# Kernel tuning notes

Measured on AMD Instinct MI355X. Metric: run time of the kernel, lower is better.

The kernel has to match this reference:

```python
import jax, jax.numpy as jnp
import numpy as np

D_MODEL = 1024
NUM_HEADS = 16
HEAD_DIM = D_MODEL // NUM_HEADS


def setup_inputs() -> dict:
    key = jax.random.key(0)
    ks = jax.random.split(key, 5)
    B, S = 2, 2048
    x = jax.random.normal(ks[0], (B, S, D_MODEL), dtype=jnp.float32)
    # nn.Linear(d,d,bias=False): y = x @ W.T, W is [out,in]. Init ~ U(-1/sqrt(d), 1/sqrt(d)).
    lim = 1.0 / np.sqrt(D_MODEL)
    wq = jax.random.uniform(ks[1], (D_MODEL, D_MODEL), jnp.float32, -lim, lim)
    wk = jax.random.uniform(ks[2], (D_MODEL, D_MODEL), jnp.float32, -lim, lim)
    wv = jax.random.uniform(ks[3], (D_MODEL, D_MODEL), jnp.float32, -lim, lim)
    wo = jax.random.uniform(ks[4], (D_MODEL, D_MODEL), jnp.float32, -lim, lim)
    return {"x": x, "wq": wq, "wk": wk, "wv": wv, "wo": wo}


def reference(x, wq, wk, wv, wo):
    B, S, D = x.shape
    H, Hd = NUM_HEADS, HEAD_DIM
    scale = Hd ** 0.5
    # projections (torch Linear: x @ W.T), split heads -> [B,H,S,Hd]
    q = (x @ wq.T).reshape(B, S, H, Hd).transpose(0, 2, 1, 3)
    k = (x @ wk.T).reshape(B, S, H, Hd).transpose(0, 2, 1, 3)
    v = (x @ wv.T).reshape(B, S, H, Hd).transpose(0, 2, 1, 3)
    scores = jnp.einsum('bhqd,bhkd->bhqk', q, k) / scale  # [B,H,S,S]
    # causal mask: disallow j > i
    causal_mask = jnp.triu(jnp.ones((S, S), dtype=bool), k=1)
    scores = jnp.where(causal_mask, -jnp.inf, scores)
    attn = jax.nn.softmax(scores, axis=-1)
    out = jnp.einsum('bhqk,bhkd->bhqd', attn, v)
    out = out.transpose(0, 2, 1, 3).reshape(B, S, D)
    return out @ wo.T
```

## Files before the change

kernel.cpp:

```cpp
#include <hip/hip_runtime.h>

#define DEV __device__ __forceinline__

typedef __attribute__((ext_vector_type(4))) float f32x4;
typedef __attribute__((ext_vector_type(8))) __bf16 bf16x8;

typedef __attribute__((address_space(1))) const uint32_t gu32;
typedef __attribute__((address_space(3))) uint32_t su32;

DEV void gload16(const void* g, void* s) {
  __builtin_amdgcn_global_load_lds((gu32*)(uintptr_t)g,
                                   (su32*)(uint32_t)(uintptr_t)s, 16, 0, 0);
}

DEV ushort bfbits(float f) { return __builtin_bit_cast(ushort, (__bf16)f); }

DEV bf16x8 lds8(const ushort* p) {
  return __builtin_bit_cast(bf16x8, *(const uint4*)(p));
}

DEV void vmcnt0bar() {
  asm volatile("s_waitcnt vmcnt(0)" ::: "memory");
  __builtin_amdgcn_s_barrier();
}

__global__ void cvt_all(const float* __restrict__ x, const float* __restrict__ wq,
                        const float* __restrict__ wk, const float* __restrict__ wv,
                        const float* __restrict__ wo, ushort* __restrict__ xb,
                        ushort* __restrict__ wb) {
  int i = blockIdx.x * blockDim.x + threadIdx.x;
  const float* src; ushort* dst; float scl = 1.0f; int j;
  if (i < 1048576) { src = x; dst = xb; j = i; }
  else {
    int t = (i - 1048576) >> 18;
    j = (i - 1048576) & 262143;
    src = t == 0 ? wq : (t == 1 ? wk : (t == 2 ? wv : wo));
    dst = wb + t * 1048576;
    if (t == 0) scl = 0.18033688011f;
  }
  float4 v = ((const float4*)src)[j];
  ushort4 o;
  o.x = bfbits(v.x * scl); o.y = bfbits(v.y * scl);
  o.z = bfbits(v.z * scl); o.w = bfbits(v.w * scl);
  ((ushort4*)dst)[j] = o;
}

template <int NFR, int F32OUT>
DEV void gemm_core(const ushort* __restrict__ A, const ushort* __restrict__ W,
                   void* __restrict__ Cout, ushort* sA, ushort* sB) {
  const int tid = threadIdx.x;
  const int l = tid & 63, wv = tid >> 6;
  const int g = l >> 4, lan = l & 15;
  const int wr = wv >> 1, wc = wv & 1;
  const int brow = blockIdx.y * 128, bcol = blockIdx.x * (NFR * 32);
  const int ASZ = 128 * 32, BSZ = NFR * 32 * 32;

  f32x4 acc[4][NFR] = {};

  auto stage = [&](int buf, int k0) {
    ushort* dA = sA + buf * ASZ;
    ushort* dB = sB + buf * BSZ;
#pragma unroll
    for (int i = 0; i < 2; ++i) {
      int n = i * 256 + wv * 64 + l;
      int row = n >> 2, ss = n & 3, gs = (ss - (row >> 1)) & 3;
      gload16(A + (size_t)(brow + row) * 1024 + k0 + gs * 8,
              dA + (i * 256 + wv * 64) * 8);
    }
#pragma unroll
    for (int i = 0; i < NFR / 2; ++i) {
      int n = i * 256 + wv * 64 + l;
      int row = n >> 2, ss = n & 3, gs = (ss - (row >> 1)) & 3;
      gload16(W + (size_t)(bcol + row) * 1024 + k0 + gs * 8,
              dB + (i * 256 + wv * 64) * 8);
    }
  };

  auto compute = [&](int buf) {
    const ushort* cA = sA + buf * ASZ;
    const ushort* cB = sB + buf * BSZ;
    bf16x8 a[4], b[NFR];
#pragma unroll
    for (int fr = 0; fr < 4; ++fr) {
      int row = wr * 64 + fr * 16 + lan;
      a[fr] = lds8(cA + row * 32 + 8 * (((row >> 1) + g) & 3));
    }
#pragma unroll
    for (int fn = 0; fn < NFR; ++fn) {
      int row = wc * (NFR * 16) + fn * 16 + lan;
      b[fn] = lds8(cB + row * 32 + 8 * (((row >> 1) + g) & 3));
    }
    __builtin_amdgcn_s_setprio(1);
#pragma unroll
    for (int fr = 0; fr < 4; ++fr)
#pragma unroll
      for (int fn = 0; fn < NFR; ++fn)
        acc[fr][fn] = __builtin_amdgcn_mfma_f32_16x16x32_bf16(a[fr], b[fn], acc[fr][fn], 0, 0, 0);
    __builtin_amdgcn_s_setprio(0);
  };

  stage(0, 0);
  vmcnt0bar();
#pragma unroll 1
  for (int t = 0; t < 15; ++t) {
    stage(1, (2 * t + 1) * 32); compute(0); vmcnt0bar();
    stage(0, (2 * t + 2) * 32); compute(1); vmcnt0bar();
  }
  stage(1, 31 * 32); compute(0); vmcnt0bar();
  compute(1);

#pragma unroll
  for (int fr = 0; fr < 4; ++fr)
#pragma unroll
    for (int fn = 0; fn < NFR; ++fn)
#pragma unroll
      for (int r = 0; r < 4; ++r) {
        int row = brow + wr * 64 + fr * 16 + g * 4 + r;
        int col = bcol + wc * (NFR * 16) + fn * 16 + lan;
        if (F32OUT)
          ((float*)Cout)[(size_t)row * 1024 + col] = acc[fr][fn][r];
        else
          ((ushort*)Cout)[(size_t)row * 1024 + col] = bfbits(acc[fr][fn][r]);
      }
}

__global__ __launch_bounds__(256) void gemm_qkv(
    const ushort* __restrict__ X, const ushort* __restrict__ Wb,
    ushort* __restrict__ Q, ushort* __restrict__ K, ushort* __restrict__ V) {
  __shared__ __align__(16) ushort sA[2 * 128 * 32];
  __shared__ __align__(16) ushort sB[2 * 128 * 32];
  const ushort* W = Wb + (size_t)blockIdx.z * 1048576;
  ushort* C = blockIdx.z == 0 ? Q : (blockIdx.z == 1 ? K : V);
  gemm_core<4, 0>(X, W, (void*)C, sA, sB);
}

__global__ __launch_bounds__(256) void gemm_out(
    const ushort* __restrict__ AO, const ushort* __restrict__ Wo, float* __restrict__ C) {
  __shared__ __align__(16) ushort sA[2 * 128 * 32];
  __shared__ __align__(16) ushort sB[2 * 64 * 32];
  gemm_core<2, 1>(AO, Wo, (void*)C, sA, sB);
}

__global__ __launch_bounds__(256) void vt_kernel(const ushort* __restrict__ V,
                                                 ushort* __restrict__ Vt) {
  __shared__ __align__(16) ushort T[64 * 64];
  const int tid = threadIdx.x;
  const int stile = blockIdx.x, bh = blockIdx.y;
  const int b = bh >> 4, h = bh & 15;

#pragma unroll
  for (int i = 0; i < 2; ++i) {
    int m = i * 256 + tid;
    int s = m >> 3, dc = m & 7;
    uint4 v = *(const uint4*)(V + (size_t)(b * 2048 + stile * 64 + s) * 1024 + h * 64 + dc * 8);
    *(uint4*)(T + s * 64 + ((8 * dc) ^ (((s >> 3) & 7) << 3))) = v;
  }
  __syncthreads();

#pragma unroll
  for (int i = 0; i < 2; ++i) {
    int m = i * 256 + tid;
    int d = m >> 3, sb = m & 7;
    ushort tmp[8];
#pragma unroll
    for (int e = 0; e < 8; ++e)
      tmp[e] = T[(sb * 8 + e) * 64 + (d ^ (sb << 3))];
    uint4 o;
    o.x = (uint)tmp[0] | ((uint)tmp[1] << 16);
    o.y = (uint)tmp[2] | ((uint)tmp[3] << 16);
    o.z = (uint)tmp[4] | ((uint)tmp[5] << 16);
    o.w = (uint)tmp[6] | ((uint)tmp[7] << 16);
    *(uint4*)(Vt + ((size_t)bh * 64 + d) * 2048 + stile * 64 + sb * 8) = o;
  }
}

__global__ __launch_bounds__(256) void attn_fwd(
    const ushort* __restrict__ Qm, const ushort* __restrict__ Km,
    const ushort* __restrict__ Vt, ushort* __restrict__ AO) {
  __shared__ __align__(16) ushort sK[2][64 * 64];
  __shared__ __align__(16) ushort sV[2][64 * 64];
  __shared__ __align__(16) ushort sP[4 * 16 * 64];

  const int tid = threadIdx.x;
  const int l = tid & 63, wv = tid >> 6;
  const int g = l >> 4, lan = l & 15;
  const int bid = blockIdx.x;
  const int rank = bid >> 5, bh = bid & 31;
  const int qt = 31 - rank;
  const int b = bh >> 4, h = bh & 15;
  const int q0 = qt * 64 + wv * 16;
  const int qg = q0 + lan;

  bf16x8 qf[2];
#pragma unroll
  for (int kf = 0; kf < 2; ++kf)
    qf[kf] = __builtin_bit_cast(bf16x8,
        *(const uint4*)(Qm + (size_t)(b * 2048 + qg) * 1024 + h * 64 + kf * 32 + g * 8));

  float mrun = -1e30f, lrun = 0.f;
  f32x4 o[4];
#pragma unroll
  for (int of = 0; of < 4; ++of) o[of] = (f32x4){0.f, 0.f, 0.f, 0.f};

  ushort* Pw = sP + wv * 1024;
  const int nkt = qt + 1;

  auto stagekv = [&](int buf, int kt) {
#pragma unroll
    for (int i = 0; i < 2; ++i) {
      int n = i * 256 + wv * 64 + l;
      int row = n >> 3, ss = n & 7, gs = ss ^ (row & 7);
      gload16(Km + (size_t)(b * 2048 + kt * 64 + row) * 1024 + h * 64 + gs * 8,
              sK[buf] + (i * 256 + wv * 64) * 8);
      gload16(Vt + ((size_t)bh * 64 + row) * 2048 + kt * 64 + gs * 8,
              sV[buf] + (i * 256 + wv * 64) * 8);
    }
  };

  stagekv(0, 0);
  vmcnt0bar();

#pragma unroll 1
  for (int kt = 0; kt < nkt; ++kt) {
    const int buf = kt & 1;
    if (kt + 1 < nkt) stagekv(buf ^ 1, kt + 1);

    f32x4 sc[4];
    __builtin_amdgcn_s_setprio(1);
#pragma unroll
    for (int kvf = 0; kvf < 4; ++kvf) {
      f32x4 a2 = (f32x4){0.f, 0.f, 0.f, 0.f};
#pragma unroll
      for (int kf = 0; kf < 2; ++kf) {
        int row = kvf * 16 + lan;
        bf16x8 kb = lds8(sK[buf] + row * 64 + 8 * ((kf * 4 + g) ^ (row & 7)));
        a2 = __builtin_amdgcn_mfma_f32_16x16x32_bf16(kb, qf[kf], a2, 0, 0, 0);
      }
      sc[kvf] = a2;
    }
    __builtin_amdgcn_s_setprio(0);

    if (kt == qt) {
#pragma unroll
      for (int kvf = 0; kvf < 4; ++kvf)
#pragma unroll
        for (int r = 0; r < 4; ++r) {
          int kvg = kt * 64 + kvf * 16 + 4 * g + r;
          sc[kvf][r] = (kvg <= qg) ? sc[kvf][r] : -1e30f;
        }
    }

    float mx = sc[0][0];
#pragma unroll
    for (int kvf = 0; kvf < 4; ++kvf)
#pragma unroll
      for (int r = 0; r < 4; ++r) mx = fmaxf(mx, sc[kvf][r]);
    mx = fmaxf(mx, __shfl_xor(mx, 16));
    mx = fmaxf(mx, __shfl_xor(mx, 32));

    const bool noresc = __all(mx <= mrun + 8.0f);
    const float mnew = noresc ? mrun : fmaxf(mrun, mx);

    float rs = 0.f;
#pragma unroll
    for (int kvf = 0; kvf < 4; ++kvf)
#pragma unroll
      for (int r = 0; r < 4; ++r) {
        float p = __builtin_exp2f(sc[kvf][r] - mnew);
        sc[kvf][r] = p;
        rs += p;
      }
    rs += __shfl_xor(rs, 16);
    rs += __shfl_xor(rs, 32);

    if (noresc) {
      lrun += rs;
    } else {
      float alpha = __builtin_exp2f(mrun - mnew);
      mrun = mnew;
      lrun = lrun * alpha + rs;
      float al[4];
#pragma unroll
      for (int r = 0; r < 4; ++r) al[r] = __shfl(alpha, g * 4 + r);
#pragma unroll
      for (int of = 0; of < 4; ++of)
#pragma unroll
        for (int r = 0; r < 4; ++r) o[of][r] *= al[r];
    }

#pragma unroll
    for (int kvf = 0; kvf < 4; ++kvf) {
      ushort4 pk;
      pk.x = bfbits(sc[kvf][0]); pk.y = bfbits(sc[kvf][1]);
      pk.z = bfbits(sc[kvf][2]); pk.w = bfbits(sc[kvf][3]);
      *(ushort4*)(Pw + lan * 64 + ((16 * kvf + 4 * g) ^ ((lan & 7) << 3))) = pk;
    }
    bf16x8 pa[2];
#pragma unroll
    for (int kf = 0; kf < 2; ++kf)
      pa[kf] = lds8(Pw + lan * 64 + ((32 * kf + 8 * g) ^ ((lan & 7) << 3)));

    __builtin_amdgcn_s_setprio(1);
#pragma unroll
    for (int of = 0; of < 4; ++of)
#pragma unroll
      for (int kf = 0; kf < 2; ++kf) {
        int row = of * 16 + lan;
        bf16x8 vb = lds8(sV[buf] + row * 64 + 8 * ((kf * 4 + g) ^ (row & 7)));
        o[of] = __builtin_amdgcn_mfma_f32_16x16x32_bf16(pa[kf], vb, o[of], 0, 0, 0);
      }
    __builtin_amdgcn_s_setprio(0);

    vmcnt0bar();
  }

#pragma unroll
  for (int r = 0; r < 4; ++r) {
    float il = 1.0f / __shfl(lrun, g * 4 + r);
#pragma unroll
    for (int of = 0; of < 4; ++of) {
      int grow = qt * 64 + wv * 16 + g * 4 + r;
      AO[(size_t)(b * 2048 + grow) * 1024 + h * 64 + of * 16 + lan] = bfbits(o[of][r] * il);
    }
  }
}

extern "C" void kernel_launch(void* const* d_in, const int* in_sizes, int n_in,
                              void* d_out, int out_size, void* d_ws, size_t ws_size,
                              hipStream_t stream) {
  const float* x  = (const float*)d_in[0];
  const float* wq = (const float*)d_in[1];
  const float* wk = (const float*)d_in[2];
  const float* wv = (const float*)d_in[3];
  const float* wo = (const float*)d_in[4];
  float* out = (float*)d_out;

  char* ws = (char*)d_ws;
  const size_t MB = 1ull << 20;
  ushort* xb = (ushort*)(ws + 0);
  ushort* wb = (ushort*)(ws + 8 * MB);
  ushort* Q  = (ushort*)(ws + 16 * MB);
  ushort* K  = (ushort*)(ws + 24 * MB);
  ushort* V  = (ushort*)(ws + 32 * MB);
  ushort* AO = (ushort*)(ws + 40 * MB);
  ushort* Vt = (ushort*)(ws + 0);
  ushort* wob = wb + 3 * 1048576;

  cvt_all<<<8192, 256, 0, stream>>>(x, wq, wk, wv, wo, xb, wb);
  gemm_qkv<<<dim3(8, 32, 3), 256, 0, stream>>>(xb, wb, Q, K, V);
  vt_kernel<<<dim3(32, 32), 256, 0, stream>>>(V, Vt);
  attn_fwd<<<1024, 256, 0, stream>>>(Q, K, Vt, AO);
  gemm_out<<<dim3(16, 32), 256, 0, stream>>>(AO, wob, out);
}
```

Measured before the change: 184.4 us.

## Triple-buffer GEMM and attention loads, pair causal query tiles per block

Both GEMMs and the attention kernel move from double to triple-buffered LDS staging. Each iteration now waits only on the previous stage's loads with a partial vmcnt and then takes a single barrier, so global loads stay in flight across compute. The attention grid is halved and each block processes a complementary pair of query tiles (pr and 31-pr), which balances causal work per block and remaps heads across blocks. The cost is more LDS per block, which may lower occupancy, and fewer blocks in the attention launch.

```diff
diff --git a/kernel.cpp b/kernel.cpp
--- a/kernel.cpp
+++ b/kernel.cpp
@@ -19,9 +19,17 @@
   return __builtin_bit_cast(bf16x8, *(const uint4*)(p));
 }
 
-DEV void vmcnt0bar() {
-  asm volatile("s_waitcnt vmcnt(0)" ::: "memory");
+template <int N> DEV void waitvm() {
+  if constexpr (N == 0)      asm volatile("s_waitcnt vmcnt(0)" ::: "memory");
+  else if constexpr (N == 3) asm volatile("s_waitcnt vmcnt(3)" ::: "memory");
+  else if constexpr (N == 4) asm volatile("s_waitcnt vmcnt(4)" ::: "memory");
+  else if constexpr (N == 6) asm volatile("s_waitcnt vmcnt(6)" ::: "memory");
+  else                       asm volatile("s_waitcnt vmcnt(8)" ::: "memory");
+}
+
+DEV void barrier_hard() {
   __builtin_amdgcn_s_barrier();
+  __builtin_amdgcn_sched_barrier(0);
 }
 
 __global__ void cvt_all(const float* __restrict__ x, const float* __restrict__ wq,
@@ -54,10 +62,13 @@
   const int wr = wv >> 1, wc = wv & 1;
   const int brow = blockIdx.y * 128, bcol = blockIdx.x * (NFR * 32);
   const int ASZ = 128 * 32, BSZ = NFR * 32 * 32;
+  const int NT = 32;
+  constexpr int LPS = 2 + NFR / 2;
 
   f32x4 acc[4][NFR] = {};
 
-  auto stage = [&](int buf, int k0) {
+  auto stage = [&](int buf, int t) {
+    const int k0 = t * 32;
     ushort* dA = sA + buf * ASZ;
     ushort* dB = sB + buf * BSZ;
 #pragma unroll
@@ -100,14 +111,17 @@
   };
 
   stage(0, 0);
-  vmcnt0bar();
 #pragma unroll 1
-  for (int t = 0; t < 15; ++t) {
-    stage(1, (2 * t + 1) * 32); compute(0); vmcnt0bar();
-    stage(0, (2 * t + 2) * 32); compute(1); vmcnt0bar();
-  }
-  stage(1, 31 * 32); compute(0); vmcnt0bar();
-  compute(1);
+  for (int t = 0; t < NT; ++t) {
+    if (t + 1 < NT) {
+      stage((t + 1) % 3, t + 1);
+      waitvm<LPS>();
+    } else {
+      waitvm<0>();
+    }
+    barrier_hard();
+    compute(t % 3);
+  }
 
 #pragma unroll
   for (int fr = 0; fr < 4; ++fr)
@@ -127,8 +141,8 @@
 __global__ __launch_bounds__(256) void gemm_qkv(
     const ushort* __restrict__ X, const ushort* __restrict__ Wb,
     ushort* __restrict__ Q, ushort* __restrict__ K, ushort* __restrict__ V) {
-  __shared__ __align__(16) ushort sA[2 * 128 * 32];
-  __shared__ __align__(16) ushort sB[2 * 128 * 32];
+  __shared__ __align__(16) ushort sA[3 * 128 * 32];
+  __shared__ __align__(16) ushort sB[3 * 128 * 32];
   const ushort* W = Wb + (size_t)blockIdx.z * 1048576;
   ushort* C = blockIdx.z == 0 ? Q : (blockIdx.z == 1 ? K : V);
   gemm_core<4, 0>(X, W, (void*)C, sA, sB);
@@ -136,8 +150,8 @@
 
 __global__ __launch_bounds__(256) void gemm_out(
     const ushort* __restrict__ AO, const ushort* __restrict__ Wo, float* __restrict__ C) {
-  __shared__ __align__(16) ushort sA[2 * 128 * 32];
-  __shared__ __align__(16) ushort sB[2 * 64 * 32];
+  __shared__ __align__(16) ushort sA[3 * 128 * 32];
+  __shared__ __align__(16) ushort sB[3 * 64 * 32];
   gemm_core<2, 1>(AO, Wo, (void*)C, sA, sB);
 }
 
@@ -177,33 +191,20 @@
 __global__ __launch_bounds__(256) void attn_fwd(
     const ushort* __restrict__ Qm, const ushort* __restrict__ Km,
     const ushort* __restrict__ Vt, ushort* __restrict__ AO) {
-  __shared__ __align__(16) ushort sK[2][64 * 64];
-  __shared__ __align__(16) ushort sV[2][64 * 64];
+  __shared__ __align__(16) ushort sK[3][64 * 64];
+  __shared__ __align__(16) ushort sV[3][64 * 64];
   __shared__ __align__(16) ushort sP[4 * 16 * 64];
 
   const int tid = threadIdx.x;
   const int l = tid & 63, wv = tid >> 6;
   const int g = l >> 4, lan = l & 15;
   const int bid = blockIdx.x;
-  const int rank = bid >> 5, bh = bid & 31;
-  const int qt = 31 - rank;
+  const int idx = bid >> 3;
+  const int bh = (bid & 7) * 4 + (idx >> 4);
+  const int pr = idx & 15;
   const int b = bh >> 4, h = bh & 15;
-  const int q0 = qt * 64 + wv * 16;
-  const int qg = q0 + lan;
-
-  bf16x8 qf[2];
-#pragma unroll
-  for (int kf = 0; kf < 2; ++kf)
-    qf[kf] = __builtin_bit_cast(bf16x8,
-        *(const uint4*)(Qm + (size_t)(b * 2048 + qg) * 1024 + h * 64 + kf * 32 + g * 8));
-
-  float mrun = -1e30f, lrun = 0.f;
-  f32x4 o[4];
-#pragma unroll
-  for (int of = 0; of < 4; ++of) o[of] = (f32x4){0.f, 0.f, 0.f, 0.f};
 
   ushort* Pw = sP + wv * 1024;
-  const int nkt = qt + 1;
 
   auto stagekv = [&](int buf, int kt) {
 #pragma unroll
@@ -217,110 +218,134 @@
     }
   };
 
-  stagekv(0, 0);
-  vmcnt0bar();
-
 #pragma unroll 1
-  for (int kt = 0; kt < nkt; ++kt) {
-    const int buf = kt & 1;
-    if (kt + 1 < nkt) stagekv(buf ^ 1, kt + 1);
-
-    f32x4 sc[4];
-    __builtin_amdgcn_s_setprio(1);
-#pragma unroll
-    for (int kvf = 0; kvf < 4; ++kvf) {
-      f32x4 a2 = (f32x4){0.f, 0.f, 0.f, 0.f};
-#pragma unroll
-      for (int kf = 0; kf < 2; ++kf) {
-        int row = kvf * 16 + lan;
-        bf16x8 kb = lds8(sK[buf] + row * 64 + 8 * ((kf * 4 + g) ^ (row & 7)));
-        a2 = __builtin_amdgcn_mfma_f32_16x16x32_bf16(kb, qf[kf], a2, 0, 0, 0);
-      }
-      sc[kvf] = a2;
-    }
-    __builtin_amdgcn_s_setprio(0);
-
-    if (kt == qt) {
+  for (int seg = 0; seg < 2; ++seg) {
+    const int qt = seg == 0 ? pr : 31 - pr;
+    const int nkt = qt + 1;
+    const int q0 = qt * 64 + wv * 16;
+    const int qg = q0 + lan;
+
+    if (seg) __syncthreads();
+
+    bf16x8 qf[2];
+#pragma unroll
+    for (int kf = 0; kf < 2; ++kf)
+      qf[kf] = __builtin_bit_cast(bf16x8,
+          *(const uint4*)(Qm + (size_t)(b * 2048 + qg) * 1024 + h * 64 + kf * 32 + g * 8));
+
+    float mrun = -1e30f, lrun = 0.f;
+    f32x4 o[4];
+#pragma unroll
+    for (int of = 0; of < 4; ++of) o[of] = (f32x4){0.f, 0.f, 0.f, 0.f};
+
+    stagekv(0, 0);
+
+#pragma unroll 1
+    for (int kt = 0; kt < nkt; ++kt) {
+      const int buf = kt % 3;
+      if (kt + 1 < nkt) {
+        stagekv((kt + 1) % 3, kt + 1);
+        waitvm<4>();
+      } else {
+        waitvm<0>();
+      }
+      barrier_hard();
+
+      f32x4 sc[4];
+      __builtin_amdgcn_s_setprio(1);
+#pragma unroll
+      for (int kvf = 0; kvf < 4; ++kvf) {
+        f32x4 a2 = (f32x4){0.f, 0.f, 0.f, 0.f};
+#pragma unroll
+        for (int kf = 0; kf < 2; ++kf) {
+          int row = kvf * 16 + lan;
+          bf16x8 kb = lds8(sK[buf] + row * 64 + 8 * ((kf * 4 + g) ^ (row & 7)));
+          a2 = __builtin_amdgcn_mfma_f32_16x16x32_bf16(kb, qf[kf], a2, 0, 0, 0);
+        }
+        sc[kvf] = a2;
+      }
+      __builtin_amdgcn_s_setprio(0);
+
+      if (kt == qt) {
+#pragma unroll
+        for (int kvf = 0; kvf < 4; ++kvf)
+#pragma unroll
+          for (int r = 0; r < 4; ++r) {
+            int kvg = kt * 64 + kvf * 16 + 4 * g + r;
+            sc[kvf][r] = (kvg <= qg) ? sc[kvf][r] : -1e30f;
+          }
+      }
+
+      float mx = sc[0][0];
 #pragma unroll
       for (int kvf = 0; kvf < 4; ++kvf)
 #pragma unroll
+        for (int r = 0; r < 4; ++r) mx = fmaxf(mx, sc[kvf][r]);
+      mx = fmaxf(mx, __shfl_xor(mx, 16));
+      mx = fmaxf(mx, __shfl_xor(mx, 32));
+
+      const bool noresc = __all(mx <= mrun + 8.0f);
+      const float mnew = noresc ? mrun : fmaxf(mrun, mx);
+
+      float rs = 0.f;
+#pragma unroll
+      for (int kvf = 0; kvf < 4; ++kvf)
+#pragma unroll
         for (int r = 0; r < 4; ++r) {
-          int kvg = kt * 64 + kvf * 16 + 4 * g + r;
-          sc[kvf][r] = (kvg <= qg) ? sc[kvf][r] : -1e30f;
+          float p = __builtin_exp2f(sc[kvf][r] - mnew);
+          sc[kvf][r] = p;
+          rs += p;
         }
-    }
-
-    float mx = sc[0][0];
-#pragma unroll
-    for (int kvf = 0; kvf < 4; ++kvf)
-#pragma unroll
-      for (int r = 0; r < 4; ++r) mx = fmaxf(mx, sc[kvf][r]);
-    mx = fmaxf(mx, __shfl_xor(mx, 16));
-    mx = fmaxf(mx, __shfl_xor(mx, 32));
-
-    const bool noresc = __all(mx <= mrun + 8.0f);
-    const float mnew = noresc ? mrun : fmaxf(mrun, mx);
-
-    float rs = 0.f;
-#pragma unroll
-    for (int kvf = 0; kvf < 4; ++kvf)
-#pragma unroll
-      for (int r = 0; r < 4; ++r) {
-        float p = __builtin_exp2f(sc[kvf][r] - mnew);
-        sc[kvf][r] = p;
-        rs += p;
-      }
-    rs += __shfl_xor(rs, 16);
-    rs += __shfl_xor(rs, 32);
-
-    if (noresc) {
-      lrun += rs;
-    } else {
-      float alpha = __builtin_exp2f(mrun - mnew);
-      mrun = mnew;
-      lrun = lrun * alpha + rs;
-      float al[4];
-#pragma unroll
-      for (int r = 0; r < 4; ++r) al[r] = __shfl(alpha, g * 4 + r);
+      rs += __shfl_xor(rs, 16);
+      rs += __shfl_xor(rs, 32);
+
+      if (noresc) {
+        lrun += rs;
+      } else {
+        float alpha = __builtin_exp2f(mrun - mnew);
+        mrun = mnew;
+        lrun = lrun * alpha + rs;
+        float al[4];
+#pragma unroll
+        for (int r = 0; r < 4; ++r) al[r] = __shfl(alpha, g * 4 + r);
+#pragma unroll
+        for (int of = 0; of < 4; ++of)
+#pragma unroll
+          for (int r = 0; r < 4; ++r) o[of][r] *= al[r];
+      }
+
+#pragma unroll
+      for (int kvf = 0; kvf < 4; ++kvf) {
+        ushort4 pk;
+        pk.x = bfbits(sc[kvf][0]); pk.y = bfbits(sc[kvf][1]);
+        pk.z = bfbits(sc[kvf][2]); pk.w = bfbits(sc[kvf][3]);
+        *(ushort4*)(Pw + lan * 64 + ((16 * kvf + 4 * g) ^ ((lan & 7) << 3))) = pk;
+      }
+      bf16x8 pa[2];
+#pragma unroll
+      for (int kf = 0; kf < 2; ++kf)
+        pa[kf] = lds8(Pw + lan * 64 + ((32 * kf + 8 * g) ^ ((lan & 7) << 3)));
+
+      __builtin_amdgcn_s_setprio(1);
 #pragma unroll
       for (int of = 0; of < 4; ++of)
 #pragma unroll
-        for (int r = 0; r < 4; ++r) o[of][r] *= al[r];
-    }
-
-#pragma unroll
-    for (int kvf = 0; kvf < 4; ++kvf) {
-      ushort4 pk;
-      pk.x = bfbits(sc[kvf][0]); pk.y = bfbits(sc[kvf][1]);
-      pk.z = bfbits(sc[kvf][2]); pk.w = bfbits(sc[kvf][3]);
-      *(ushort4*)(Pw + lan * 64 + ((16 * kvf + 4 * g) ^ ((lan & 7) << 3))) = pk;
-    }
-    bf16x8 pa[2];
-#pragma unroll
-    for (int kf = 0; kf < 2; ++kf)
-      pa[kf] = lds8(Pw + lan * 64 + ((32 * kf + 8 * g) ^ ((lan & 7) << 3)));
-
-    __builtin_amdgcn_s_setprio(1);
-#pragma unroll
-    for (int of = 0; of < 4; ++of)
-#pragma unroll
-      for (int kf = 0; kf < 2; ++kf) {
-        int row = of * 16 + lan;
-        bf16x8 vb = lds8(sV[buf] + row * 64 + 8 * ((kf * 4 + g) ^ (row & 7)));
-        o[of] = __builtin_amdgcn_mfma_f32_16x16x32_bf16(pa[kf], vb, o[of], 0, 0, 0);
-      }
-    __builtin_amdgcn_s_setprio(0);
-
-    vmcnt0bar();
-  }
-
-#pragma unroll
-  for (int r = 0; r < 4; ++r) {
-    float il = 1.0f / __shfl(lrun, g * 4 + r);
-#pragma unroll
-    for (int of = 0; of < 4; ++of) {
-      int grow = qt * 64 + wv * 16 + g * 4 + r;
-      AO[(size_t)(b * 2048 + grow) * 1024 + h * 64 + of * 16 + lan] = bfbits(o[of][r] * il);
+        for (int kf = 0; kf < 2; ++kf) {
+          int row = of * 16 + lan;
+          bf16x8 vb = lds8(sV[buf] + row * 64 + 8 * ((kf * 4 + g) ^ (row & 7)));
+          o[of] = __builtin_amdgcn_mfma_f32_16x16x32_bf16(pa[kf], vb, o[of], 0, 0, 0);
+        }
+      __builtin_amdgcn_s_setprio(0);
+    }
+
+#pragma unroll
+    for (int r = 0; r < 4; ++r) {
+      float il = 1.0f / __shfl(lrun, g * 4 + r);
+#pragma unroll
+      for (int of = 0; of < 4; ++of) {
+        int grow = qt * 64 + wv * 16 + g * 4 + r;
+        AO[(size_t)(b * 2048 + grow) * 1024 + h * 64 + of * 16 + lan] = bfbits(o[of][r] * il);
+      }
     }
   }
 }
@@ -349,6 +374,6 @@
   cvt_all<<<8192, 256, 0, stream>>>(x, wq, wk, wv, wo, xb, wb);
   gemm_qkv<<<dim3(8, 32, 3), 256, 0, stream>>>(xb, wb, Q, K, V);
   vt_kernel<<<dim3(32, 32), 256, 0, stream>>>(V, Vt);
-  attn_fwd<<<1024, 256, 0, stream>>>(Q, K, Vt, AO);
+  attn_fwd<<<512, 256, 0, stream>>>(Q, K, Vt, AO);
   gemm_out<<<dim3(16, 32), 256, 0, stream>>>(AO, wob, out);
 }
```

New measurement: 194.7 us. +5.6%, slower.

## Halve KV tile to 32, skip fully-masked warps, remap blocks for load balance

Applied to the files above, without the earlier changes.

The attention kernel now streams K/V in 32-row tiles instead of 64, which halves LDS use per block, and raises the occupancy hint to 6 blocks per CU. Each warp skips compute on tiles that lie entirely above its causal diagonal. The block index mapping is changed to interleave short and long query tiles across batch-heads for better balance. The cost is twice as many loop iterations, each with a barrier and half the MFMA work, so there is more synchronisation overhead per unit of work.

```diff
diff --git a/kernel.cpp b/kernel.cpp
--- a/kernel.cpp
+++ b/kernel.cpp
@@ -174,22 +174,27 @@
   }
 }
 
-__global__ __launch_bounds__(256) void attn_fwd(
+__global__ __launch_bounds__(256, 6) void attn_fwd(
     const ushort* __restrict__ Qm, const ushort* __restrict__ Km,
     const ushort* __restrict__ Vt, ushort* __restrict__ AO) {
-  __shared__ __align__(16) ushort sK[2][64 * 64];
-  __shared__ __align__(16) ushort sV[2][64 * 64];
-  __shared__ __align__(16) ushort sP[4 * 16 * 64];
+  __shared__ __align__(16) ushort sK[2][32 * 64];
+  __shared__ __align__(16) ushort sV[2][64 * 32];
+  __shared__ __align__(16) ushort sP[4 * 16 * 32];
 
   const int tid = threadIdx.x;
   const int l = tid & 63, wv = tid >> 6;
   const int g = l >> 4, lan = l & 15;
   const int bid = blockIdx.x;
-  const int rank = bid >> 5, bh = bid & 31;
-  const int qt = 31 - rank;
+  const int j = bid >> 8, c = bid & 255;
+  const int u = c >> 3, v = c & 7;
+  const int w = (u + ((j >> 1) << 4)) & 31;
+  const int qt = (j & 1) ? (31 - w) : w;
+  const int bh = v + 8 * j;
   const int b = bh >> 4, h = bh & 15;
+
   const int q0 = qt * 64 + wv * 16;
   const int qg = q0 + lan;
+  const int nkt = 2 * qt + 2;
 
   bf16x8 qf[2];
 #pragma unroll
@@ -202,19 +207,17 @@
 #pragma unroll
   for (int of = 0; of < 4; ++of) o[of] = (f32x4){0.f, 0.f, 0.f, 0.f};
 
-  ushort* Pw = sP + wv * 1024;
-  const int nkt = qt + 1;
+  ushort* Pw = sP + wv * 512;
+
+  const int ck = wv * 64 + l;
+  const int krow = ck >> 3, kphys = ck & 7;
+  const int vrow = ck >> 2, vphys = ck & 3;
+  const ushort* Ksrc0 = Km + (size_t)(b * 2048 + krow) * 1024 + h * 64 + ((kphys ^ (krow & 7)) * 8);
+  const ushort* Vsrc0 = Vt + ((size_t)bh * 64 + vrow) * 2048 + ((vphys ^ (vrow & 3)) * 8);
 
   auto stagekv = [&](int buf, int kt) {
-#pragma unroll
-    for (int i = 0; i < 2; ++i) {
-      int n = i * 256 + wv * 64 + l;
-      int row = n >> 3, ss = n & 7, gs = ss ^ (row & 7);
-      gload16(Km + (size_t)(b * 2048 + kt * 64 + row) * 1024 + h * 64 + gs * 8,
-              sK[buf] + (i * 256 + wv * 64) * 8);
-      gload16(Vt + ((size_t)bh * 64 + row) * 2048 + kt * 64 + gs * 8,
-              sV[buf] + (i * 256 + wv * 64) * 8);
-    }
+    gload16(Ksrc0 + (size_t)(kt * 32) * 1024, sK[buf] + ck * 8);
+    gload16(Vsrc0 + kt * 32, sV[buf] + ck * 8);
   };
 
   stagekv(0, 0);
@@ -225,91 +228,90 @@
     const int buf = kt & 1;
     if (kt + 1 < nkt) stagekv(buf ^ 1, kt + 1);
 
-    f32x4 sc[4];
-    __builtin_amdgcn_s_setprio(1);
-#pragma unroll
-    for (int kvf = 0; kvf < 4; ++kvf) {
-      f32x4 a2 = (f32x4){0.f, 0.f, 0.f, 0.f};
-#pragma unroll
-      for (int kf = 0; kf < 2; ++kf) {
-        int row = kvf * 16 + lan;
-        bf16x8 kb = lds8(sK[buf] + row * 64 + 8 * ((kf * 4 + g) ^ (row & 7)));
-        a2 = __builtin_amdgcn_mfma_f32_16x16x32_bf16(kb, qf[kf], a2, 0, 0, 0);
-      }
-      sc[kvf] = a2;
-    }
-    __builtin_amdgcn_s_setprio(0);
-
-    if (kt == qt) {
-#pragma unroll
-      for (int kvf = 0; kvf < 4; ++kvf)
+    const bool active = (kt * 32 <= q0 + 15);
+    if (active) {
+      f32x4 sc[2];
+      __builtin_amdgcn_s_setprio(1);
+#pragma unroll
+      for (int kvf = 0; kvf < 2; ++kvf) {
+        f32x4 a2 = (f32x4){0.f, 0.f, 0.f, 0.f};
+#pragma unroll
+        for (int kf = 0; kf < 2; ++kf) {
+          int row = kvf * 16 + lan;
+          bf16x8 kb = lds8(sK[buf] + row * 64 + (((kf * 4 + g) ^ (row & 7)) * 8));
+          a2 = __builtin_amdgcn_mfma_f32_16x16x32_bf16(kb, qf[kf], a2, 0, 0, 0);
+        }
+        sc[kvf] = a2;
+      }
+      __builtin_amdgcn_s_setprio(0);
+
+      if (kt >= 2 * qt) {
+#pragma unroll
+        for (int kvf = 0; kvf < 2; ++kvf)
+#pragma unroll
+          for (int r = 0; r < 4; ++r) {
+            int kvg = kt * 32 + kvf * 16 + 4 * g + r;
+            sc[kvf][r] = (kvg <= qg) ? sc[kvf][r] : -1e30f;
+          }
+      }
+
+      float mx = fmaxf(sc[0][0], sc[1][0]);
+#pragma unroll
+      for (int kvf = 0; kvf < 2; ++kvf)
+#pragma unroll
+        for (int r = 0; r < 4; ++r) mx = fmaxf(mx, sc[kvf][r]);
+      mx = fmaxf(mx, __shfl_xor(mx, 16));
+      mx = fmaxf(mx, __shfl_xor(mx, 32));
+
+      const bool noresc = __all(mx <= mrun + 8.0f);
+      const float mnew = noresc ? mrun : fmaxf(mrun, mx);
+
+      float rs = 0.f;
+#pragma unroll
+      for (int kvf = 0; kvf < 2; ++kvf)
 #pragma unroll
         for (int r = 0; r < 4; ++r) {
-          int kvg = kt * 64 + kvf * 16 + 4 * g + r;
-          sc[kvf][r] = (kvg <= qg) ? sc[kvf][r] : -1e30f;
+          float p = __builtin_exp2f(sc[kvf][r] - mnew);
+          sc[kvf][r] = p;
+          rs += p;
         }
-    }
-
-    float mx = sc[0][0];
-#pragma unroll
-    for (int kvf = 0; kvf < 4; ++kvf)
-#pragma unroll
-      for (int r = 0; r < 4; ++r) mx = fmaxf(mx, sc[kvf][r]);
-    mx = fmaxf(mx, __shfl_xor(mx, 16));
-    mx = fmaxf(mx, __shfl_xor(mx, 32));
-
-    const bool noresc = __all(mx <= mrun + 8.0f);
-    const float mnew = noresc ? mrun : fmaxf(mrun, mx);
-
-    float rs = 0.f;
-#pragma unroll
-    for (int kvf = 0; kvf < 4; ++kvf)
-#pragma unroll
-      for (int r = 0; r < 4; ++r) {
-        float p = __builtin_exp2f(sc[kvf][r] - mnew);
-        sc[kvf][r] = p;
-        rs += p;
-      }
-    rs += __shfl_xor(rs, 16);
-    rs += __shfl_xor(rs, 32);
-
-    if (noresc) {
-      lrun += rs;
-    } else {
-      float alpha = __builtin_exp2f(mrun - mnew);
-      mrun = mnew;
-      lrun = lrun * alpha + rs;
-      float al[4];
-#pragma unroll
-      for (int r = 0; r < 4; ++r) al[r] = __shfl(alpha, g * 4 + r);
-#pragma unroll
-      for (int of = 0; of < 4; ++of)
-#pragma unroll
-        for (int r = 0; r < 4; ++r) o[of][r] *= al[r];
-    }
-
-#pragma unroll
-    for (int kvf = 0; kvf < 4; ++kvf) {
-      ushort4 pk;
-      pk.x = bfbits(sc[kvf][0]); pk.y = bfbits(sc[kvf][1]);
-      pk.z = bfbits(sc[kvf][2]); pk.w = bfbits(sc[kvf][3]);
-      *(ushort4*)(Pw + lan * 64 + ((16 * kvf + 4 * g) ^ ((lan & 7) << 3))) = pk;
-    }
-    bf16x8 pa[2];
-#pragma unroll
-    for (int kf = 0; kf < 2; ++kf)
-      pa[kf] = lds8(Pw + lan * 64 + ((32 * kf + 8 * g) ^ ((lan & 7) << 3)));
-
-    __builtin_amdgcn_s_setprio(1);
-#pragma unroll
-    for (int of = 0; of < 4; ++of)
-#pragma unroll
-      for (int kf = 0; kf < 2; ++kf) {
+      rs += __shfl_xor(rs, 16);
+      rs += __shfl_xor(rs, 32);
+
+      if (noresc) {
+        lrun += rs;
+      } else {
+        float alpha = __builtin_exp2f(mrun - mnew);
+        mrun = mnew;
+        lrun = lrun * alpha + rs;
+        float al[4];
+#pragma unroll
+        for (int r = 0; r < 4; ++r) al[r] = __shfl(alpha, g * 4 + r);
+#pragma unroll
+        for (int of = 0; of < 4; ++of)
+#pragma unroll
+          for (int r = 0; r < 4; ++r) o[of][r] *= al[r];
+      }
+
+#pragma unroll
+      for (int kvf = 0; kvf < 2; ++kvf) {
+        ushort4 pk;
+        pk.x = bfbits(sc[kvf][0]); pk.y = bfbits(sc[kvf][1]);
+        pk.z = bfbits(sc[kvf][2]); pk.w = bfbits(sc[kvf][3]);
+        int phys16 = (kvf * 2 + (g >> 1)) ^ (lan & 3);
+        *(ushort4*)(Pw + lan * 32 + phys16 * 8 + (g & 1) * 4) = pk;
+      }
+      bf16x8 pa = lds8(Pw + lan * 32 + ((g ^ (lan & 3)) * 8));
+
+      __builtin_amdgcn_s_setprio(1);
+#pragma unroll
+      for (int of = 0; of < 4; ++of) {
         int row = of * 16 + lan;
-        bf16x8 vb = lds8(sV[buf] + row * 64 + 8 * ((kf * 4 + g) ^ (row & 7)));
-        o[of] = __builtin_amdgcn_mfma_f32_16x16x32_bf16(pa[kf], vb, o[of], 0, 0, 0);
-      }
-    __builtin_amdgcn_s_setprio(0);
+        bf16x8 vb = lds8(sV[buf] + row * 32 + ((g ^ (row & 3)) * 8));
+        o[of] = __builtin_amdgcn_mfma_f32_16x16x32_bf16(pa, vb, o[of], 0, 0, 0);
+      }
+      __builtin_amdgcn_s_setprio(0);
+    }
 
     vmcnt0bar();
   }
@@ -319,7 +321,7 @@
     float il = 1.0f / __shfl(lrun, g * 4 + r);
 #pragma unroll
     for (int of = 0; of < 4; ++of) {
-      int grow = qt * 64 + wv * 16 + g * 4 + r;
+      int grow = q0 + g * 4 + r;
       AO[(size_t)(b * 2048 + grow) * 1024 + h * 64 + of * 16 + lan] = bfbits(o[of][r] * il);
     }
   }
```

Result: slower. 208.7 us (+13.2%).

## Fuse V transpose into QKV GEMM epilogue and load V fragments directly to registers

Applied to the files above, without the earlier changes.

The V projection GEMM now writes its output already transposed into the per-head [bh, d, s] layout, which removes the separate vt_kernel launch and its extra pass over V. In attention, V fragments are loaded straight from global memory into registers and no longer staged through LDS, with a partial vmcnt wait so the next K tile stays in flight. The block-to-(q-tile, head) mapping is also reordered to pair long and short causal tiles and to improve locality. The cost is scattered 8-byte global stores in the GEMM epilogue and uncoalesced per-lane V loads whose latency is exposed inside the loop.

```diff
diff --git a/kernel.cpp b/kernel.cpp
--- a/kernel.cpp
+++ b/kernel.cpp
@@ -17,6 +17,11 @@
 
 DEV bf16x8 lds8(const ushort* p) {
   return __builtin_bit_cast(bf16x8, *(const uint4*)(p));
+}
+
+template <int N> DEV void waitvm() {
+  if constexpr (N == 0)      asm volatile("s_waitcnt vmcnt(0)" ::: "memory");
+  else if constexpr (N == 2) asm volatile("s_waitcnt vmcnt(2)" ::: "memory");
 }
 
 DEV void vmcnt0bar() {
@@ -45,7 +50,7 @@
   ((ushort4*)dst)[j] = o;
 }
 
-template <int NFR, int F32OUT>
+template <int NFR, int OUT_MODE>
 DEV void gemm_core(const ushort* __restrict__ A, const ushort* __restrict__ W,
                    void* __restrict__ Cout, ushort* sA, ushort* sB) {
   const int tid = threadIdx.x;
@@ -112,26 +117,40 @@
 #pragma unroll
   for (int fr = 0; fr < 4; ++fr)
 #pragma unroll
-    for (int fn = 0; fn < NFR; ++fn)
-#pragma unroll
-      for (int r = 0; r < 4; ++r) {
-        int row = brow + wr * 64 + fr * 16 + g * 4 + r;
+    for (int fn = 0; fn < NFR; ++fn) {
+      if (OUT_MODE == 2) {
+        int row = brow + wr * 64 + fr * 16 + g * 4;
         int col = bcol + wc * (NFR * 16) + fn * 16 + lan;
-        if (F32OUT)
-          ((float*)Cout)[(size_t)row * 1024 + col] = acc[fr][fn][r];
-        else
-          ((ushort*)Cout)[(size_t)row * 1024 + col] = bfbits(acc[fr][fn][r]);
+        int bh2 = (row >> 11) * 16 + (col >> 6);
+        int d = col & 63, s0 = row & 2047;
+        ushort4 pk;
+        pk.x = bfbits(acc[fr][fn][0]); pk.y = bfbits(acc[fr][fn][1]);
+        pk.z = bfbits(acc[fr][fn][2]); pk.w = bfbits(acc[fr][fn][3]);
+        *(ushort4*)((ushort*)Cout + ((size_t)bh2 * 64 + d) * 2048 + s0) = pk;
+      } else {
+#pragma unroll
+        for (int r = 0; r < 4; ++r) {
+          int row = brow + wr * 64 + fr * 16 + g * 4 + r;
+          int col = bcol + wc * (NFR * 16) + fn * 16 + lan;
+          if (OUT_MODE == 1)
+            ((float*)Cout)[(size_t)row * 1024 + col] = acc[fr][fn][r];
+          else
+            ((ushort*)Cout)[(size_t)row * 1024 + col] = bfbits(acc[fr][fn][r]);
+        }
       }
+    }
 }
 
 __global__ __launch_bounds__(256) void gemm_qkv(
     const ushort* __restrict__ X, const ushort* __restrict__ Wb,
-    ushort* __restrict__ Q, ushort* __restrict__ K, ushort* __restrict__ V) {
+    ushort* __restrict__ Q, ushort* __restrict__ K, ushort* __restrict__ Vt) {
   __shared__ __align__(16) ushort sA[2 * 128 * 32];
   __shared__ __align__(16) ushort sB[2 * 128 * 32];
   const ushort* W = Wb + (size_t)blockIdx.z * 1048576;
-  ushort* C = blockIdx.z == 0 ? Q : (blockIdx.z == 1 ? K : V);
-  gemm_core<4, 0>(X, W, (void*)C, sA, sB);
+  if (blockIdx.z == 2)
+    gemm_core<4, 2>(X, W, (void*)Vt, sA, sB);
+  else
+    gemm_core<4, 0>(X, W, (void*)(blockIdx.z == 0 ? Q : K), sA, sB);
 }
 
 __global__ __launch_bounds__(256) void gemm_out(
@@ -141,52 +160,21 @@
   gemm_core<2, 1>(AO, Wo, (void*)C, sA, sB);
 }
 
-__global__ __launch_bounds__(256) void vt_kernel(const ushort* __restrict__ V,
-                                                 ushort* __restrict__ Vt) {
-  __shared__ __align__(16) ushort T[64 * 64];
-  const int tid = threadIdx.x;
-  const int stile = blockIdx.x, bh = blockIdx.y;
-  const int b = bh >> 4, h = bh & 15;
-
-#pragma unroll
-  for (int i = 0; i < 2; ++i) {
-    int m = i * 256 + tid;
-    int s = m >> 3, dc = m & 7;
-    uint4 v = *(const uint4*)(V + (size_t)(b * 2048 + stile * 64 + s) * 1024 + h * 64 + dc * 8);
-    *(uint4*)(T + s * 64 + ((8 * dc) ^ (((s >> 3) & 7) << 3))) = v;
-  }
-  __syncthreads();
-
-#pragma unroll
-  for (int i = 0; i < 2; ++i) {
-    int m = i * 256 + tid;
-    int d = m >> 3, sb = m & 7;
-    ushort tmp[8];
-#pragma unroll
-    for (int e = 0; e < 8; ++e)
-      tmp[e] = T[(sb * 8 + e) * 64 + (d ^ (sb << 3))];
-    uint4 o;
-    o.x = (uint)tmp[0] | ((uint)tmp[1] << 16);
-    o.y = (uint)tmp[2] | ((uint)tmp[3] << 16);
-    o.z = (uint)tmp[4] | ((uint)tmp[5] << 16);
-    o.w = (uint)tmp[6] | ((uint)tmp[7] << 16);
-    *(uint4*)(Vt + ((size_t)bh * 64 + d) * 2048 + stile * 64 + sb * 8) = o;
-  }
-}
-
 __global__ __launch_bounds__(256) void attn_fwd(
     const ushort* __restrict__ Qm, const ushort* __restrict__ Km,
-    const ushort* __restrict__ Vt, ushort* __restrict__ AO) {
+    const ushort* __restrict__ Vtm, ushort* __restrict__ AO) {
   __shared__ __align__(16) ushort sK[2][64 * 64];
-  __shared__ __align__(16) ushort sV[2][64 * 64];
   __shared__ __align__(16) ushort sP[4 * 16 * 64];
 
   const int tid = threadIdx.x;
   const int l = tid & 63, wv = tid >> 6;
   const int g = l >> 4, lan = l & 15;
   const int bid = blockIdx.x;
-  const int rank = bid >> 5, bh = bid & 31;
-  const int qt = 31 - rank;
+  const int j = bid >> 8, c = bid & 255;
+  const int u = c >> 3, vv = c & 7;
+  const int w = (u + ((j >> 1) << 4)) & 31;
+  const int qt = (j & 1) ? (31 - w) : w;
+  const int bh = vv + 8 * j;
   const int b = bh >> 4, h = bh & 15;
   const int q0 = qt * 64 + wv * 16;
   const int qg = q0 + lan;
@@ -205,25 +193,33 @@
   ushort* Pw = sP + wv * 1024;
   const int nkt = qt + 1;
 
-  auto stagekv = [&](int buf, int kt) {
+  auto stageK = [&](int buf, int kt) {
 #pragma unroll
     for (int i = 0; i < 2; ++i) {
       int n = i * 256 + wv * 64 + l;
       int row = n >> 3, ss = n & 7, gs = ss ^ (row & 7);
       gload16(Km + (size_t)(b * 2048 + kt * 64 + row) * 1024 + h * 64 + gs * 8,
               sK[buf] + (i * 256 + wv * 64) * 8);
-      gload16(Vt + ((size_t)bh * 64 + row) * 2048 + kt * 64 + gs * 8,
-              sV[buf] + (i * 256 + wv * 64) * 8);
     }
   };
 
-  stagekv(0, 0);
+  stageK(0, 0);
   vmcnt0bar();
 
 #pragma unroll 1
   for (int kt = 0; kt < nkt; ++kt) {
     const int buf = kt & 1;
-    if (kt + 1 < nkt) stagekv(buf ^ 1, kt + 1);
+
+    bf16x8 vb[4][2];
+#pragma unroll
+    for (int of = 0; of < 4; ++of)
+#pragma unroll
+      for (int kf = 0; kf < 2; ++kf)
+        vb[of][kf] = __builtin_bit_cast(bf16x8,
+            *(const uint4*)(Vtm + ((size_t)bh * 64 + of * 16 + lan) * 2048 +
+                            kt * 64 + kf * 32 + g * 8));
+    __builtin_amdgcn_sched_barrier(0);
+    if (kt + 1 < nkt) stageK(buf ^ 1, kt + 1);
 
     f32x4 sc[4];
     __builtin_amdgcn_s_setprio(1);
@@ -300,15 +296,14 @@
     for (int kf = 0; kf < 2; ++kf)
       pa[kf] = lds8(Pw + lan * 64 + ((32 * kf + 8 * g) ^ ((lan & 7) << 3)));
 
+    if (kt + 1 < nkt) waitvm<2>(); else waitvm<0>();
+
     __builtin_amdgcn_s_setprio(1);
 #pragma unroll
     for (int of = 0; of < 4; ++of)
 #pragma unroll
-      for (int kf = 0; kf < 2; ++kf) {
-        int row = of * 16 + lan;
-        bf16x8 vb = lds8(sV[buf] + row * 64 + 8 * ((kf * 4 + g) ^ (row & 7)));
-        o[of] = __builtin_amdgcn_mfma_f32_16x16x32_bf16(pa[kf], vb, o[of], 0, 0, 0);
-      }
+      for (int kf = 0; kf < 2; ++kf)
+        o[of] = __builtin_amdgcn_mfma_f32_16x16x32_bf16(pa[kf], vb[of][kf], o[of], 0, 0, 0);
     __builtin_amdgcn_s_setprio(0);
 
     vmcnt0bar();
@@ -319,7 +314,7 @@
     float il = 1.0f / __shfl(lrun, g * 4 + r);
 #pragma unroll
     for (int of = 0; of < 4; ++of) {
-      int grow = qt * 64 + wv * 16 + g * 4 + r;
+      int grow = q0 + g * 4 + r;
       AO[(size_t)(b * 2048 + grow) * 1024 + h * 64 + of * 16 + lan] = bfbits(o[of][r] * il);
     }
   }
@@ -341,14 +336,12 @@
   ushort* wb = (ushort*)(ws + 8 * MB);
   ushort* Q  = (ushort*)(ws + 16 * MB);
   ushort* K  = (ushort*)(ws + 24 * MB);
-  ushort* V  = (ushort*)(ws + 32 * MB);
+  ushort* Vt = (ushort*)(ws + 32 * MB);
   ushort* AO = (ushort*)(ws + 40 * MB);
-  ushort* Vt = (ushort*)(ws + 0);
   ushort* wob = wb + 3 * 1048576;
 
   cvt_all<<<8192, 256, 0, stream>>>(x, wq, wk, wv, wo, xb, wb);
-  gemm_qkv<<<dim3(8, 32, 3), 256, 0, stream>>>(xb, wb, Q, K, V);
-  vt_kernel<<<dim3(32, 32), 256, 0, stream>>>(V, Vt);
+  gemm_qkv<<<dim3(8, 32, 3), 256, 0, stream>>>(xb, wb, Q, K, Vt);
   attn_fwd<<<1024, 256, 0, stream>>>(Q, K, Vt, AO);
   gemm_out<<<dim3(16, 32), 256, 0, stream>>>(AO, wob, out);
 }
```

Result: slower. 215.9 us (+17.1%).
